# Optimization experiments

Measured on AMD Instinct MI355X. Metric: run time of the kernel, lower is better.

## Reference

```python
import jax, jax.numpy as jnp
import numpy as np

K = 3
STRIDE = 1
PAD = 1


def _conv(x, w, b):
    y = jax.lax.conv_general_dilated(
        x, w, window_strides=(STRIDE, STRIDE),
        padding=[(PAD, PAD), (PAD, PAD)],
        dimension_numbers=('NCHW', 'OIHW', 'NCHW'))
    return y + b[None, :, None, None]


def setup_inputs() -> dict:
    key = jax.random.key(0)
    ks = jax.random.split(key, 6)
    B, Cin, H, W = 4, 64, 128, 128
    Cout = 128
    x = jax.random.normal(ks[0], (B, Cin, H, W), dtype=jnp.float32)
    # small random offset/mask conv params (original inits to 0, which would be degenerate)
    w_off = jax.random.normal(ks[1], (2 * K * K, Cin, K, K), dtype=jnp.float32) * 0.01
    b_off = jax.random.normal(ks[2], (2 * K * K,), dtype=jnp.float32) * 0.1
    w_mask = jax.random.normal(ks[3], (K * K, Cin, K, K), dtype=jnp.float32) * 0.01
    b_mask = jnp.zeros((K * K,), dtype=jnp.float32)
    # kaiming_uniform(a=sqrt(5)) -> bound = 1/sqrt(fan_in)
    fan_in = Cin * K * K
    bound = 1.0 / np.sqrt(fan_in)
    weight = jax.random.uniform(ks[4], (Cout, Cin, K, K), dtype=jnp.float32,
                                minval=-bound, maxval=bound)
    return {"x": x, "w_off": w_off, "b_off": b_off,
            "w_mask": w_mask, "b_mask": b_mask, "weight": weight}


def _deform_conv(x, offset, mask, weight):
    B, C, H, W = x.shape
    O = weight.shape[0]
    KK = K * K
    Ho, Wo = offset.shape[2], offset.shape[3]
    # torchvision layout: offset[:, 2k] = dy_k, offset[:, 2k+1] = dx_k
    off = offset.reshape(B, KK, 2, Ho, Wo)
    dy, dx = off[:, :, 0], off[:, :, 1]  # [B,KK,Ho,Wo]

    ky, kx = jnp.meshgrid(jnp.arange(K), jnp.arange(K), indexing='ij')
    ky = ky.reshape(KK).astype(jnp.float32)
    kx = kx.reshape(KK).astype(jnp.float32)
    oy = jnp.arange(Ho, dtype=jnp.float32) * STRIDE - PAD
    ox = jnp.arange(Wo, dtype=jnp.float32) * STRIDE - PAD
    # sampling positions [B,KK,Ho,Wo]
    py = oy[None, None, :, None] + ky[None, :, None, None] + dy
    px = ox[None, None, None, :] + kx[None, :, None, None] + dx

    y0 = jnp.floor(py)
    x0 = jnp.floor(px)
    ly = py - y0
    lx = px - x0
    y0i = y0.astype(jnp.int32)
    x0i = x0.astype(jnp.int32)

    x_flat = x.reshape(B, C, H * W)
    gather = jax.vmap(lambda xf, idx: xf[:, idx])  # ([C,HW],[KK,Ho,Wo])->[C,KK,Ho,Wo]

    def corner(yi, xi, wgt):
        valid = ((yi >= 0) & (yi < H) & (xi >= 0) & (xi < W)).astype(x.dtype)
        yc = jnp.clip(yi, 0, H - 1)
        xc = jnp.clip(xi, 0, W - 1)
        g = gather(x_flat, yc * W + xc)  # [B,C,KK,Ho,Wo]
        return g * (wgt * valid)[:, None]

    sampled = (corner(y0i, x0i, (1 - ly) * (1 - lx))
               + corner(y0i, x0i + 1, (1 - ly) * lx)
               + corner(y0i + 1, x0i, ly * (1 - lx))
               + corner(y0i + 1, x0i + 1, ly * lx))  # [B,C,KK,Ho,Wo]

    sampled = sampled * mask[:, None]  # modulation, mask [B,KK,Ho,Wo]
    w = weight.reshape(O, C, KK)
    return jnp.einsum('bckhw,ock->bohw', sampled, w)


def reference(x, w_off, b_off, w_mask, b_mask, weight):
    offset = _conv(x, w_off, b_off)
    mask = jax.nn.sigmoid(_conv(x, w_mask, b_mask))
    return _deform_conv(x, offset, mask, weight)
```

## Files before the change

kernel.cpp:

```cpp
#include <hip/hip_runtime.h>
#include <math.h>

#define B 4
#define CIN 64
#define H 128
#define W 128
#define COUT 128
#define KK 9
#define HW (H*W)

#define WBF_COLS 640
#define WBF_SHORTS (COUT*WBF_COLS)
#define WCV_SHORTS (32*640)
#define LDK 168

typedef __attribute__((ext_vector_type(8))) short short8;
typedef __attribute__((ext_vector_type(4))) float f32x4;
typedef __attribute__((ext_vector_type(2))) float f32x2;
typedef f32x2 __attribute__((aligned(4))) f32x2a;

#define GLDS16(g, l) __builtin_amdgcn_global_load_lds(                        \
    (__attribute__((address_space(1))) void*)(g),                             \
    (__attribute__((address_space(3))) void*)(l), 16, 0, 0)

__device__ __forceinline__ unsigned short f2bf(float f) {
    unsigned int u = __float_as_uint(f);
    u += 0x7fffu + ((u >> 16) & 1u);
    return (unsigned short)(u >> 16);
}

__global__ void prep_wcv(const float* __restrict__ w_off, const float* __restrict__ b_off,
                         const float* __restrict__ w_mask, const float* __restrict__ b_mask,
                         short* __restrict__ wcv, float* __restrict__ bcat)
{
    int idx = blockIdx.x * 256 + threadIdx.x;
    if (idx < WCV_SHORTS) {
        int f  = idx / 640;
        int kp = idx % 640;
        int cb = kp / 160, r = kp % 160;
        float v = 0.f;
        if (r < 144) {
            int tap = r >> 4;
            int c   = cb * 16 + (r & 15);
            if (f < 18)      v = w_off[(f * CIN + c) * 9 + tap];
            else if (f < 27) v = w_mask[((f - 18) * CIN + c) * 9 + tap];
        }
        wcv[idx] = (short)f2bf(v);
    }
    if (blockIdx.x == 0 && threadIdx.x < 32) {
        int f = threadIdx.x;
        float bv = 0.f;
        if (f < 18) bv = b_off[f];
        else if (f < 27) bv = b_mask[f - 18];
        bcat[f] = bv;
    }
}

__global__ void prep_wbf(const float* __restrict__ wgt, short* __restrict__ wbf)
{
    int idx = blockIdx.x * 256 + threadIdx.x;
    if (idx >= WBF_SHORTS) return;
    int o  = idx / WBF_COLS;
    int kp = idx % WBF_COLS;
    int cb = kp / 160, r = kp % 160;
    float v = 0.f;
    if (r < 144) {
        int tap = r >> 4;
        int c   = cb * 16 + (r & 15);
        v = wgt[(o * CIN + c) * KK + tap];
    }
    wbf[idx] = (short)f2bf(v);
}

__global__ __launch_bounds__(256, 2) void fused2_kernel(
    const float* __restrict__ x, const short* __restrict__ wcv,
    const short* __restrict__ wbf, const float* __restrict__ bcat,
    float* __restrict__ out)
{
    const int bid = blockIdx.x;
    const int T = (bid & 7) * 128 + (bid >> 3);
    const int wo0 = (T & 1) * 64;
    const int ho  = (T >> 1) & 127;
    const int b   = T >> 8;
    const int tid  = threadIdx.x;
    const int lane = tid & 63;
    const int wv   = tid >> 6;
    const int oh   = (wv & 1) * 64;
    const int ph   = (wv >> 1) * 32;
    const int row16 = lane & 15, kq = lane >> 4;

    __shared__ __align__(16) float XW[8 * 6 * 72];
    __shared__ __align__(16) short S[64 * LDK];
    float* offs_l = (float*)S;

    const float* xb = x + (size_t)b * CIN * HW;

    int stA_goff[2];
    #pragma unroll
    for (int t = 0; t < 2; ++t) {
        int idx = tid + t * 256;
        int ci = idx / 54, rem = idx % 54, row = rem / 18, q = rem % 18;
        int ys = min(max(ho - 1 + row, 0), H - 1);
        int g0 = wo0 - 4 + q * 4;
        int g0c = min(max(g0, 0), W - 4);
        stA_goff[t] = ci * HW + ys * W + g0c;
    }
    auto stageA = [&](int h) {
        const float* base = xb + (size_t)h * 8 * HW;
        #pragma unroll
        for (int t = 0; t < 2; ++t) {
            if (tid + t * 256 < 432) {
                GLDS16(base + stA_goff[t], &XW[(tid + t * 256) * 4]);
            }
        }
    };

    if (tid < 128) {
        short8 z = {0,0,0,0,0,0,0,0};
        *(short8*)&S[(tid >> 1) * LDK + 144 + (tid & 1) * 8] = z;
    }
    stageA(0);

    int bidx[3];
    #pragma unroll
    for (int j = 0; j < 3; ++j) {
        bidx[j] = -1;
        int s = tid + j * 256;
        if (s < 576) {
            int k = s >> 6, p = s & 63;
            int ky = k / 3, kx = k % 3;
            bool ok = ((unsigned)(ho - 1 + ky) < (unsigned)H)
                   && ((unsigned)(wo0 + p - 1 + kx) < (unsigned)W);
            if (ok) bidx[j] = ky * 72 + (p + 3 + kx);
        }
    }
    int stB_goff[4];
    #pragma unroll
    for (int t = 0; t < 4; ++t) {
        int idx = tid + t * 256;
        int ci = idx / 108, rem = idx % 108, row = rem / 18, q = rem % 18;
        int ys = min(max(ho - 2 + row, 0), H - 1);
        int g0 = wo0 - 4 + q * 4;
        int g0c = min(max(g0, 0), W - 4);
        stB_goff[t] = ci * HW + ys * W + g0c;
    }
    __syncthreads();

    f32x4 acc2[2];
    acc2[0] = (f32x4){0.f, 0.f, 0.f, 0.f};
    acc2[1] = (f32x4){0.f, 0.f, 0.f, 0.f};

    auto buildA = [&](int h) {
        #pragma unroll
        for (int j = 0; j < 3; ++j) {
            int s = tid + j * 256;
            if (s < 576) {
                int k = s >> 6, p = s & 63;
                short8 sv = {0,0,0,0,0,0,0,0};
                if (bidx[j] >= 0) {
                    #pragma unroll
                    for (int ci = 0; ci < 8; ++ci)
                        sv[ci] = (short)f2bf(XW[ci * 216 + bidx[j]]);
                }
                *(short8*)&S[p * LDK + k * 16 + (h & 1) * 8] = sv;
            }
        }
    };
    auto mfmaA = [&](int c) {
        #pragma unroll
        for (int ks = 0; ks < 5; ++ks) {
            short8 a0 = *(const short8*)(wcv + (row16)      * 640 + c * 160 + ks * 32 + kq * 8);
            short8 a1 = *(const short8*)(wcv + (16 + row16) * 640 + c * 160 + ks * 32 + kq * 8);
            short8 bfr = *(const short8*)&S[(wv * 16 + row16) * LDK + ks * 32 + kq * 8];
            acc2[0] = __builtin_amdgcn_mfma_f32_16x16x32_bf16(a0, bfr, acc2[0], 0, 0, 0);
            acc2[1] = __builtin_amdgcn_mfma_f32_16x16x32_bf16(a1, bfr, acc2[1], 0, 0, 0);
        }
    };

    buildA(0); __syncthreads();
    stageA(1); __syncthreads(); buildA(1); __syncthreads();
    #pragma unroll 1
    for (int c = 0; c < 3; ++c) {
        stageA(2 * c + 2);
        mfmaA(c);
        __syncthreads();
        buildA(2 * c + 2);
        __syncthreads();
        stageA(2 * c + 3);
        __syncthreads();
        buildA(2 * c + 3);
        __syncthreads();
    }
    mfmaA(3);
    __syncthreads();

    {
        const int pxl = wv * 16 + row16;
        #pragma unroll
        for (int of = 0; of < 2; ++of) {
            #pragma unroll
            for (int r = 0; r < 4; ++r) {
                int f = of * 16 + kq * 4 + r;
                if (f < 27) {
                    float v = acc2[of][r] + bcat[f];
                    if (f >= 18) v = 1.f / (1.f + expf(-v));
                    offs_l[f * 64 + pxl] = v;
                }
            }
        }
    }
    __syncthreads();

    auto stageB = [&](int h) {
        const float* base = xb + (size_t)h * 8 * HW;
        #pragma unroll
        for (int t = 0; t < 4; ++t) {
            if (tid + t * 256 < 864) {
                GLDS16(base + stB_goff[t], &XW[(tid + t * 256) * 4]);
            }
        }
    };

    stageB(0);

    int   moff[3][2];
    int   lidx0[3], lidx1[3];
    f32x2 wAB[3], wCD[3];
    #pragma unroll
    for (int j = 0; j < 3; ++j) {
        moff[j][0] = 0; moff[j][1] = 0;
        lidx0[j] = -1; lidx1[j] = 0;
        wAB[j] = (f32x2){0.f, 0.f}; wCD[j] = (f32x2){0.f, 0.f};
        int s = tid + j * 256;
        if (s < 576) {
            int k = s >> 6, p = s & 63;
            int wo = wo0 + p;
            int ky = k / 3, kx = k % 3;
            float dy = offs_l[(2 * k) * 64 + p];
            float dx = offs_l[(2 * k + 1) * 64 + p];
            float mk = offs_l[(18 + k) * 64 + p];
            float py  = (float)(ho - 1 + ky) + dy;
            float pxf = (float)(wo - 1 + kx) + dx;
            float fy = floorf(py), fx = floorf(pxf);
            float ly = py - fy, lx = pxf - fx;
            int y0 = (int)fy, x0 = (int)fx;
            int y1 = y0 + 1,  x1 = x0 + 1;
            bool vy0 = (y0 >= 0) && (y0 < H);
            bool vy1 = (y1 >= 0) && (y1 < H);
            bool vx0 = (x0 >= 0) && (x0 < W);
            bool vx1 = (x1 >= 0) && (x1 < W);
            float w0 = (vy0 && vx0) ? (1.f - ly) * (1.f - lx) * mk : 0.f;
            float w1 = (vy0 && vx1) ? (1.f - ly) * lx * mk : 0.f;
            float w2 = (vy1 && vx0) ? ly * (1.f - lx) * mk : 0.f;
            float w3 = (vy1 && vx1) ? ly * lx * mk : 0.f;
            int lc = min(max(x0, 0), W - 2);
            bool sel = (x0 == lc);
            int r0 = min(max(y0, 0), H - 1);
            int r1 = min(max(y1, 0), H - 1);
            moff[j][0] = (r0 * W + lc) * 4;
            moff[j][1] = (r1 * W + lc) * 4;
            wAB[j].x = sel ? w0 : w1;  wAB[j].y = sel ? w1 : w0;
            wCD[j].x = sel ? w2 : w3;  wCD[j].y = sel ? w3 : w2;
            int u0 = r0 - (ho - 2);
            int u1 = r1 - (ho - 2);
            int vvv = lc - (wo0 - 4);
            bool fastp = ((unsigned)u0 < 6u) && ((unsigned)u1 < 6u)
                       && ((unsigned)vvv < 71u);
            lidx1[j] = u1 * 72 + vvv;
            lidx0[j] = fastp ? (u0 * 72 + vvv) : -1;
        }
    }
    __syncthreads();

    if (tid < 128) {
        short8 z = {0,0,0,0,0,0,0,0};
        *(short8*)&S[(tid >> 1) * LDK + 144 + (tid & 1) * 8] = z;
    }

    f32x4 acc[4][2];
    #pragma unroll
    for (int i = 0; i < 4; ++i)
        #pragma unroll
        for (int j = 0; j < 2; ++j)
            acc[i][j] = (f32x4){0.f, 0.f, 0.f, 0.f};

    auto sampleB = [&](int h) {
        #pragma unroll
        for (int j = 0; j < 3; ++j) {
            int s = tid + j * 256;
            if (s < 576) {
                int k = s >> 6, p = s & 63;
                float va[8];
                f32x2 wab = wAB[j], wcd = wCD[j];
                if (lidx0[j] >= 0) {
                    int l0 = lidx0[j], l1 = lidx1[j];
                    #pragma unroll
                    for (int ci = 0; ci < 8; ++ci) {
                        const float* bp = &XW[ci * 432];
                        f32x2 A  = *(const f32x2a*)(bp + l0);
                        f32x2 Bv = *(const f32x2a*)(bp + l1);
                        f32x2 t = A * wab + Bv * wcd;
                        va[ci] = t.x + t.y;
                    }
                } else {
                    #pragma unroll
                    for (int ci = 0; ci < 8; ++ci) {
                        const char* pc = (const char*)(xb + (size_t)(h * 8 + ci) * HW);
                        f32x2 A  = *(const f32x2a*)(pc + moff[j][0]);
                        f32x2 Bv = *(const f32x2a*)(pc + moff[j][1]);
                        f32x2 t = A * wab + Bv * wcd;
                        va[ci] = t.x + t.y;
                    }
                }
                short8 sv;
                #pragma unroll
                for (int ci = 0; ci < 8; ++ci) sv[ci] = (short)f2bf(va[ci]);
                *(short8*)&S[p * LDK + k * 16 + (h & 1) * 8] = sv;
            }
        }
    };

    auto mfmaB = [&](int c) {
        #pragma unroll
        for (int ks = 0; ks < 5; ++ks) {
            short8 a[4];
            #pragma unroll
            for (int of = 0; of < 4; ++of) {
                int o = oh + of * 16 + row16;
                a[of] = *(const short8*)(wbf + o * WBF_COLS + c * 160 + ks * 32 + kq * 8);
            }
            #pragma unroll
            for (int pf = 0; pf < 2; ++pf) {
                int p = ph + pf * 16 + row16;
                short8 bfr = *(const short8*)&S[p * LDK + ks * 32 + kq * 8];
                #pragma unroll
                for (int of = 0; of < 4; ++of)
                    acc[of][pf] = __builtin_amdgcn_mfma_f32_16x16x32_bf16(
                        a[of], bfr, acc[of][pf], 0, 0, 0);
            }
        }
    };

    sampleB(0); __syncthreads();
    stageB(1); __syncthreads(); sampleB(1); __syncthreads();
    #pragma unroll 1
    for (int c = 0; c < 3; ++c) {
        stageB(2 * c + 2);
        mfmaB(c);
        __syncthreads();
        sampleB(2 * c + 2);
        __syncthreads();
        stageB(2 * c + 3);
        __syncthreads();
        sampleB(2 * c + 3);
        __syncthreads();
    }
    mfmaB(3);

    #pragma unroll
    for (int of = 0; of < 4; ++of) {
        #pragma unroll
        for (int r = 0; r < 4; ++r) {
            int o = oh + of * 16 + kq * 4 + r;
            float* orow = out + ((b * COUT + o) * H + ho) * W;
            #pragma unroll
            for (int pf = 0; pf < 2; ++pf) {
                int wo = wo0 + ph + pf * 16 + row16;
                orow[wo] = acc[of][pf][r];
            }
        }
    }
}

extern "C" void kernel_launch(void* const* d_in, const int* in_sizes, int n_in,
                              void* d_out, int out_size, void* d_ws, size_t ws_size,
                              hipStream_t stream)
{
    const float* x      = (const float*)d_in[0];
    const float* w_off  = (const float*)d_in[1];
    const float* b_off  = (const float*)d_in[2];
    const float* w_mask = (const float*)d_in[3];
    const float* b_mask = (const float*)d_in[4];
    const float* weight = (const float*)d_in[5];
    float* out   = (float*)d_out;

    float* bcat  = (float*)d_ws;
    short* wbf   = (short*)(bcat + 32);
    short* wcv   = wbf + WBF_SHORTS;

    prep_wcv<<<dim3((WCV_SHORTS + 255) / 256), 256, 0, stream>>>(
        w_off, b_off, w_mask, b_mask, wcv, bcat);
    prep_wbf<<<dim3((WBF_SHORTS + 255) / 256), 256, 0, stream>>>(weight, wbf);
    fused2_kernel<<<dim3(1024), 256, 0, stream>>>(x, wcv, wbf, bcat, out);
}
```

Before: 84.71 us.

## Stage 16 input channels per round to halve pipeline syncs

```diff
diff --git a/kernel.cpp b/kernel.cpp
--- a/kernel.cpp
+++ b/kernel.cpp
@@ -72,7 +72,7 @@
     wbf[idx] = (short)f2bf(v);
 }
 
-__global__ __launch_bounds__(256, 2) void fused2_kernel(
+__global__ __launch_bounds__(256, 2) void fused3_kernel(
     const float* __restrict__ x, const short* __restrict__ wcv,
     const short* __restrict__ wbf, const float* __restrict__ bcat,
     float* __restrict__ out)
@@ -89,15 +89,15 @@
     const int ph   = (wv >> 1) * 32;
     const int row16 = lane & 15, kq = lane >> 4;
 
-    __shared__ __align__(16) float XW[8 * 6 * 72];
+    __shared__ __align__(16) float XW[16 * 6 * 72];
     __shared__ __align__(16) short S[64 * LDK];
     float* offs_l = (float*)S;
 
     const float* xb = x + (size_t)b * CIN * HW;
 
-    int stA_goff[2];
-    #pragma unroll
-    for (int t = 0; t < 2; ++t) {
+    int stA_goff[4];
+    #pragma unroll
+    for (int t = 0; t < 4; ++t) {
         int idx = tid + t * 256;
         int ci = idx / 54, rem = idx % 54, row = rem / 18, q = rem % 18;
         int ys = min(max(ho - 1 + row, 0), H - 1);
@@ -105,11 +105,11 @@
         int g0c = min(max(g0, 0), W - 4);
         stA_goff[t] = ci * HW + ys * W + g0c;
     }
-    auto stageA = [&](int h) {
-        const float* base = xb + (size_t)h * 8 * HW;
-        #pragma unroll
-        for (int t = 0; t < 2; ++t) {
-            if (tid + t * 256 < 432) {
+    auto stageA = [&](int c) {
+        const float* base = xb + (size_t)c * 16 * HW;
+        #pragma unroll
+        for (int t = 0; t < 4; ++t) {
+            if (tid + t * 256 < 864) {
                 GLDS16(base + stA_goff[t], &XW[(tid + t * 256) * 4]);
             }
         }
@@ -134,9 +134,9 @@
             if (ok) bidx[j] = ky * 72 + (p + 3 + kx);
         }
     }
-    int stB_goff[4];
-    #pragma unroll
-    for (int t = 0; t < 4; ++t) {
+    int stB_goff[7];
+    #pragma unroll
+    for (int t = 0; t < 7; ++t) {
         int idx = tid + t * 256;
         int ci = idx / 108, rem = idx % 108, row = rem / 18, q = rem % 18;
         int ys = min(max(ho - 2 + row, 0), H - 1);
@@ -150,19 +150,22 @@
     acc2[0] = (f32x4){0.f, 0.f, 0.f, 0.f};
     acc2[1] = (f32x4){0.f, 0.f, 0.f, 0.f};
 
-    auto buildA = [&](int h) {
+    auto buildA = [&](int) {
         #pragma unroll
         for (int j = 0; j < 3; ++j) {
             int s = tid + j * 256;
             if (s < 576) {
                 int k = s >> 6, p = s & 63;
-                short8 sv = {0,0,0,0,0,0,0,0};
-                if (bidx[j] >= 0) {
-                    #pragma unroll
-                    for (int ci = 0; ci < 8; ++ci)
-                        sv[ci] = (short)f2bf(XW[ci * 216 + bidx[j]]);
+                #pragma unroll
+                for (int h2 = 0; h2 < 2; ++h2) {
+                    short8 sv = {0,0,0,0,0,0,0,0};
+                    if (bidx[j] >= 0) {
+                        #pragma unroll
+                        for (int c8 = 0; c8 < 8; ++c8)
+                            sv[c8] = (short)f2bf(XW[(h2 * 8 + c8) * 216 + bidx[j]]);
+                    }
+                    *(short8*)&S[p * LDK + k * 16 + h2 * 8] = sv;
                 }
-                *(short8*)&S[p * LDK + k * 16 + (h & 1) * 8] = sv;
             }
         }
     };
@@ -177,18 +180,14 @@
         }
     };
 
-    buildA(0); __syncthreads();
-    stageA(1); __syncthreads(); buildA(1); __syncthreads();
+    buildA(0);
+    __syncthreads();
     #pragma unroll 1
     for (int c = 0; c < 3; ++c) {
-        stageA(2 * c + 2);
+        stageA(c + 1);
         mfmaA(c);
         __syncthreads();
-        buildA(2 * c + 2);
-        __syncthreads();
-        stageA(2 * c + 3);
-        __syncthreads();
-        buildA(2 * c + 3);
+        buildA(c + 1);
         __syncthreads();
     }
     mfmaA(3);
@@ -211,11 +210,11 @@
     }
     __syncthreads();
 
-    auto stageB = [&](int h) {
-        const float* base = xb + (size_t)h * 8 * HW;
-        #pragma unroll
-        for (int t = 0; t < 4; ++t) {
-            if (tid + t * 256 < 864) {
+    auto stageB = [&](int c) {
+        const float* base = xb + (size_t)c * 16 * HW;
+        #pragma unroll
+        for (int t = 0; t < 7; ++t) {
+            if (tid + t * 256 < 1728) {
                 GLDS16(base + stB_goff[t], &XW[(tid + t * 256) * 4]);
             }
         }
@@ -284,38 +283,42 @@
         for (int j = 0; j < 2; ++j)
             acc[i][j] = (f32x4){0.f, 0.f, 0.f, 0.f};
 
-    auto sampleB = [&](int h) {
+    auto sampleB = [&](int cc) {
         #pragma unroll
         for (int j = 0; j < 3; ++j) {
             int s = tid + j * 256;
             if (s < 576) {
                 int k = s >> 6, p = s & 63;
-                float va[8];
                 f32x2 wab = wAB[j], wcd = wCD[j];
-                if (lidx0[j] >= 0) {
-                    int l0 = lidx0[j], l1 = lidx1[j];
+                #pragma unroll
+                for (int h2 = 0; h2 < 2; ++h2) {
+                    float va[8];
+                    if (lidx0[j] >= 0) {
+                        int l0 = lidx0[j], l1 = lidx1[j];
+                        #pragma unroll
+                        for (int c8 = 0; c8 < 8; ++c8) {
+                            const float* bp = &XW[(h2 * 8 + c8) * 432];
+                            f32x2 A  = *(const f32x2a*)(bp + l0);
+                            f32x2 Bv = *(const f32x2a*)(bp + l1);
+                            f32x2 t = A * wab + Bv * wcd;
+                            va[c8] = t.x + t.y;
+                        }
+                    } else {
+                        #pragma unroll
+                        for (int c8 = 0; c8 < 8; ++c8) {
+                            const char* pc = (const char*)
+                                (xb + (size_t)(cc * 16 + h2 * 8 + c8) * HW);
+                            f32x2 A  = *(const f32x2a*)(pc + moff[j][0]);
+                            f32x2 Bv = *(const f32x2a*)(pc + moff[j][1]);
+                            f32x2 t = A * wab + Bv * wcd;
+                            va[c8] = t.x + t.y;
+                        }
+                    }
+                    short8 sv;
                     #pragma unroll
-                    for (int ci = 0; ci < 8; ++ci) {
-                        const float* bp = &XW[ci * 432];
-                        f32x2 A  = *(const f32x2a*)(bp + l0);
-                        f32x2 Bv = *(const f32x2a*)(bp + l1);
-                        f32x2 t = A * wab + Bv * wcd;
-                        va[ci] = t.x + t.y;
-                    }
-                } else {
-                    #pragma unroll
-                    for (int ci = 0; ci < 8; ++ci) {
-                        const char* pc = (const char*)(xb + (size_t)(h * 8 + ci) * HW);
-                        f32x2 A  = *(const f32x2a*)(pc + moff[j][0]);
-                        f32x2 Bv = *(const f32x2a*)(pc + moff[j][1]);
-                        f32x2 t = A * wab + Bv * wcd;
-                        va[ci] = t.x + t.y;
-                    }
+                    for (int c8 = 0; c8 < 8; ++c8) sv[c8] = (short)f2bf(va[c8]);
+                    *(short8*)&S[p * LDK + k * 16 + h2 * 8] = sv;
                 }
-                short8 sv;
-                #pragma unroll
-                for (int ci = 0; ci < 8; ++ci) sv[ci] = (short)f2bf(va[ci]);
-                *(short8*)&S[p * LDK + k * 16 + (h & 1) * 8] = sv;
             }
         }
     };
@@ -341,18 +344,14 @@
         }
     };
 
-    sampleB(0); __syncthreads();
-    stageB(1); __syncthreads(); sampleB(1); __syncthreads();
+    sampleB(0);
+    __syncthreads();
     #pragma unroll 1
     for (int c = 0; c < 3; ++c) {
-        stageB(2 * c + 2);
+        stageB(c + 1);
         mfmaB(c);
         __syncthreads();
-        sampleB(2 * c + 2);
-        __syncthreads();
-        stageB(2 * c + 3);
-        __syncthreads();
-        sampleB(2 * c + 3);
+        sampleB(c + 1);
         __syncthreads();
     }
     mfmaB(3);
@@ -391,5 +390,5 @@
     prep_wcv<<<dim3((WCV_SHORTS + 255) / 256), 256, 0, stream>>>(
         w_off, b_off, w_mask, b_mask, wcv, bcat);
     prep_wbf<<<dim3((WBF_SHORTS + 255) / 256), 256, 0, stream>>>(weight, wbf);
-    fused2_kernel<<<dim3(1024), 256, 0, stream>>>(x, wcv, wbf, bcat, out);
-}
+    fused3_kernel<<<dim3(1024), 256, 0, stream>>>(x, wcv, wbf, bcat, out);
+}
```

New measurement: 103.1 us. 1.22x slower.
